# Optimization experiments

Hardware: AMD Instinct MI355X
Metric: run time of the kernel (lower is better)

## Reference

```python
import jax, jax.numpy as jnp
import numpy as np

HIDDEN = 1024
HEADS = 16
HEAD_DIM = HIDDEN // HEADS          # 64
ROT = 2 * (HEAD_DIM // 3 // 2)      # 20 (d/h/w rotary chunk), residual = 4
GRID = 256 // 16                    # crop_size // patch_size = 16
DEPTH = 16 // 2                     # frames_per_clip // tubelet_size = 8
N_VIDEO = DEPTH * GRID * GRID       # 2048
N_ACTION = 16
B = 2
SCALE = HEAD_DIM ** -0.5


def _rope(x, pos):
    # interleaved RoPE (VJEPA2 rotate_queries_or_keys): pairs (x[2i], x[2i+1])
    D = x.shape[-1]
    omega = 1.0 / (10000.0 ** (jnp.arange(D // 2, dtype=x.dtype) / (D / 2.0)))
    freq = pos.astype(x.dtype)[..., None] * omega          # (N, D/2)
    cos, sin = jnp.cos(freq), jnp.sin(freq)
    x1, x2 = x[..., 0::2], x[..., 1::2]
    return jnp.stack([x1 * cos - x2 * sin, x2 * cos + x1 * sin], axis=-1).reshape(x.shape)


def _rope3(qk, d_pos, h_pos, w_pos):
    # rotate three ROT-sized chunks (depth/height/width axes), leave residual dims as-is
    parts = [_rope(qk[..., 0:ROT], d_pos),
             _rope(qk[..., ROT:2 * ROT], h_pos),
             _rope(qk[..., 2 * ROT:3 * ROT], w_pos)]
    if 3 * ROT < HEAD_DIM:
        parts.append(qk[..., 3 * ROT:])
    return jnp.concatenate(parts, axis=-1)


def _forward(video_hidden_states, action_hidden_states, W_q, b_q, W_k, b_k, W_v, b_v,
             W_qa, b_qa, W_ka, b_ka, W_va, b_va, W_proj, b_proj, W_proj_a, b_proj_a):
    Bsz, Nv, _ = video_hidden_states.shape
    Na = action_hidden_states.shape[1]

    def proj(x, W, b):  # -> (B, H, N, Dh)
        y = x @ W.T + b
        return y.reshape(Bsz, -1, HEADS, HEAD_DIM).transpose(0, 2, 1, 3)

    qv = proj(video_hidden_states, W_q, b_q)
    kv = proj(video_hidden_states, W_k, b_k)
    vv = proj(video_hidden_states, W_v, b_v)

    # 3-axis position ids for raster-ordered video tokens
    ids = jnp.arange(Nv)
    tpf = GRID * GRID
    d_pos = ids // tpf
    rem = ids - tpf * d_pos
    h_pos = rem // GRID
    w_pos = rem - GRID * h_pos

    qv = _rope3(qv, d_pos, h_pos, w_pos)
    kv = _rope3(kv, d_pos, h_pos, w_pos)

    qa = proj(action_hidden_states, W_qa, b_qa)
    ka = proj(action_hidden_states, W_ka, b_ka)
    va = proj(action_hidden_states, W_va, b_va)

    # actions: linspace between frame-id of token 0 and token 1 (faithful to source)
    a_pos = jnp.linspace(d_pos[0].astype(jnp.float32), d_pos[1].astype(jnp.float32), Na)
    qa = _rope3(qa, a_pos, a_pos, a_pos)
    ka = _rope3(ka, a_pos, a_pos, a_pos)

    # joint attention over concatenated video+action token sequence
    q = jnp.concatenate([qv, qa], axis=2)
    k = jnp.concatenate([kv, ka], axis=2)
    v = jnp.concatenate([vv, va], axis=2)

    scores = jnp.einsum('bhqd,bhkd->bhqk', q, k) * SCALE
    probs = jax.nn.softmax(scores, axis=-1)
    ctx = jnp.einsum('bhqk,bhkd->bhqd', probs, v)
    ctx = ctx.transpose(0, 2, 1, 3).reshape(Bsz, Nv + Na, HIDDEN)

    out_video = ctx[:, :Nv] @ W_proj.T + b_proj
    out_action = ctx[:, Nv:] @ W_proj_a.T + b_proj_a
    return out_video, out_action


def setup_inputs() -> dict:
    key = jax.random.key(0)
    ks = jax.random.split(key, 12)
    sd = HIDDEN ** -0.5
    inp = {}
    for i, n in enumerate(['q', 'k', 'v', 'qa', 'ka', 'va', 'proj', 'proj_a']):
        inp[f'W_{n}'] = jax.random.normal(ks[i], (HIDDEN, HIDDEN), jnp.float32) * sd
        inp[f'b_{n}'] = jnp.zeros((HIDDEN,), jnp.float32)
    inp['video_hidden_states'] = jax.random.normal(ks[10], (B, N_VIDEO, HIDDEN), jnp.float32)
    inp['action_hidden_states'] = jax.random.normal(ks[11], (B, N_ACTION, HIDDEN), jnp.float32)
    return inp


def reference(video_hidden_states, action_hidden_states, W_q, b_q, W_k, b_k, W_v, b_v,
              W_qa, b_qa, W_ka, b_ka, W_va, b_va, W_proj, b_proj, W_proj_a, b_proj_a):
    return _forward(video_hidden_states, action_hidden_states, W_q, b_q, W_k, b_k, W_v, b_v,
                    W_qa, b_qa, W_ka, b_ka, W_va, b_va, W_proj, b_proj, W_proj_a, b_proj_a)
```

## Files before the change

### kernel.cpp

```cpp
#include <hip/hip_runtime.h>
#include <stdint.h>

#define HID   1024
#define NHEAD 16
#define HDIM  64
#define NV    2048
#define NA    16
#define NTOK  2064
#define BSZ   2
#define MROWS 4128
#define MPAD  4224
#define WSZ   1048576
#define EXP_C1 0.18033688011112042f
#define EXP_C2 16.0f

#define POFF(r,k)  (((((r)>>4)*32  + ((k)>>5))*512) + ((((k)>>3)&3)*128) + (((r)&15)*8) + ((k)&7))
#define QOFF(t,d)  (((((t)>>4)*2   + ((d)>>5))*512) + ((((d)>>3)&3)*128) + (((t)&15)*8) + ((d)&7))
#define VOFF(d,ky) (((((d)>>4)*65  + ((ky)>>5))*512) + ((((ky)>>3)&3)*128) + (((d)&15)*8) + ((ky)&7))
#define QPLANE (129*2*512)
#define VPLANE (4*65*512)

typedef __bf16 bf16x8 __attribute__((ext_vector_type(8)));
typedef unsigned short u16x8 __attribute__((ext_vector_type(8)));
typedef unsigned short u16x4 __attribute__((ext_vector_type(4)));
typedef float f32x4 __attribute__((ext_vector_type(4)));

__device__ __forceinline__ unsigned short f2bf(float f) {
  unsigned u = __builtin_bit_cast(unsigned, f);
  u += 0x7FFFu + ((u >> 16) & 1u);
  return (unsigned short)(u >> 16);
}
__device__ __forceinline__ unsigned short f2bf_trunc(float f) {
  return (unsigned short)(__builtin_bit_cast(unsigned, f) >> 16);
}
__device__ __forceinline__ bf16x8 ldfrag(const unsigned short* p) {
  return __builtin_bit_cast(bf16x8, *(const u16x8*)p);
}

__global__ __launch_bounds__(256) void cvt_kernel(
    const float* __restrict__ W0, const float* __restrict__ W1,
    const float* __restrict__ W2, const float* __restrict__ W3,
    const float* __restrict__ W4, const float* __restrict__ W5,
    const float* __restrict__ W6, const float* __restrict__ W7,
    const float* __restrict__ video, const float* __restrict__ action,
    unsigned short* __restrict__ Wb, unsigned short* __restrict__ Xp)
{
  const int y = blockIdx.y;
  const size_t idx = ((size_t)blockIdx.x * 256 + threadIdx.x) * 8;
  const float* src; unsigned short* dstbase; int row;
  if (y < 8) {
    const float* Ws[8] = {W0, W1, W2, W3, W4, W5, W6, W7};
    src = Ws[y] + idx; dstbase = Wb + (size_t)y * WSZ; row = (int)(idx >> 10);
  } else if (y < 12) {
    src = video + (size_t)(y - 8) * WSZ + idx; dstbase = Xp;
    row = ((y - 8) << 10) + (int)(idx >> 10);
  } else {
    if (idx >= (size_t)BSZ * NA * HID) return;
    src = action + idx; dstbase = Xp; row = 4096 + (int)(idx >> 10);
  }
  const int k0 = (int)(idx & 1023);
  float4 f0 = *(const float4*)src;
  float4 f1 = *(const float4*)(src + 4);
  u16x8 v;
  v[0]=f2bf(f0.x); v[1]=f2bf(f0.y); v[2]=f2bf(f0.z); v[3]=f2bf(f0.w);
  v[4]=f2bf(f1.x); v[5]=f2bf(f1.y); v[6]=f2bf(f1.z); v[7]=f2bf(f1.w);
  *(u16x8*)(dstbase + POFF(row, k0)) = v;
}

__device__ __forceinline__ void row2bt(int rg, int& b, int& tok, bool& valid) {
  if (rg < 4096) { b = rg >> 11; tok = rg & 2047; valid = true; }
  else { int t = rg - 4096; b = t >> 4; tok = 2048 + (t & 15); valid = rg < MROWS; }
}

__global__ __launch_bounds__(512) void qkv_kernel(
    const unsigned short* __restrict__ Xp, const unsigned short* __restrict__ Wb,
    const float* __restrict__ bq, const float* __restrict__ bk,
    const float* __restrict__ bv, const float* __restrict__ bqa,
    const float* __restrict__ bka, const float* __restrict__ bva,
    unsigned short* __restrict__ Qpk, unsigned short* __restrict__ Kpk,
    unsigned short* __restrict__ Vpk)
{
  const int tid  = threadIdx.x;
  const int w    = tid >> 6;
  const int lane = tid & 63;
  const int quad = lane >> 4;
  const int l16  = lane & 15;
  const int mh   = w & 3;
  const int nh   = w >> 2;
  const int n0   = blockIdx.x * 128;
  const int z    = blockIdx.y;
  const int m0   = blockIdx.z * 128;
  const bool atile = (blockIdx.z == 32);

  const unsigned short* Wz = Wb + (size_t)(atile ? 3 + z : z) * WSZ;
  const float* bias = (z == 0) ? (atile ? bqa : bq)
                    : (z == 1) ? (atile ? bka : bk)
                               : (atile ? bva : bv);

  const int Mt = (m0 >> 4) + mh * 2;
  const int Nt = (n0 >> 4) + nh * 4;
  const unsigned short* pa = Xp + (size_t)Mt * 32 * 512 + lane * 8;
  const unsigned short* pb = Wz + (size_t)Nt * 32 * 512 + lane * 8;

  f32x4 acc[2][4] = {};
  bf16x8 af[2][2], bf[2][4];

#pragma unroll
  for (int mi = 0; mi < 2; mi++) af[0][mi] = ldfrag(pa + (size_t)(mi * 32) * 512);
#pragma unroll
  for (int ni = 0; ni < 4; ni++) bf[0][ni] = ldfrag(pb + (size_t)(ni * 32) * 512);

  for (int kt = 0; kt < 32; kt++) {
    const int cb = kt & 1, nb = cb ^ 1;
    if (kt < 31) {
#pragma unroll
      for (int mi = 0; mi < 2; mi++) af[nb][mi] = ldfrag(pa + (size_t)(mi * 32 + kt + 1) * 512);
#pragma unroll
      for (int ni = 0; ni < 4; ni++) bf[nb][ni] = ldfrag(pb + (size_t)(ni * 32 + kt + 1) * 512);
    }
#pragma unroll
    for (int mi = 0; mi < 2; mi++)
#pragma unroll
      for (int ni = 0; ni < 4; ni++)
        acc[mi][ni] = __builtin_amdgcn_mfma_f32_16x16x32_bf16(af[cb][mi], bf[cb][ni], acc[mi][ni], 0, 0, 0);
  }

  if (z < 2) {
    unsigned short* O = (z == 0) ? Qpk : Kpk;
#pragma unroll
    for (int mi = 0; mi < 2; mi++) {
      const int rgb = m0 + mh * 32 + mi * 16 + quad * 4;
#pragma unroll
      for (int ni = 0; ni < 4; ni++) {
        const int gcol = n0 + nh * 64 + ni * 16 + l16;
        const int head = gcol >> 6, col = gcol & 63;
        const float bias_v = bias[gcol];
        const int seg = (col >= 40) ? 2 : (col >= 20) ? 1 : 0;
        const int tin = col - seg * 20;
        const float om = exp2f(-(float)(tin >> 1) * 1.3287712379549449f);
        const bool evn = !(tin & 1);
#pragma unroll
        for (int r = 0; r < 4; r++) {
          int rg = rgb + r;
          int b, tok; bool valid;
          row2bt(rg, b, tok, valid);
          float val = acc[mi][ni][r] + bias_v;
          float part = __shfl_xor(val, 1);
          if (tok < 2048 && col < 60) {
            int dp = tok >> 8, hp = (tok >> 4) & 15, wp = tok & 15;
            float pos = (seg == 0) ? (float)dp : (seg == 1) ? (float)hp : (float)wp;
            float fr = pos * om;
            float cs = cosf(fr), sn = sinf(fr);
            val = evn ? (val * cs - part * sn) : (val * cs + part * sn);
          }
          if (valid)
            O[(size_t)(b * NHEAD + head) * QPLANE + QOFF(tok, col)] = f2bf(val);
        }
      }
    }
  } else {
#pragma unroll
    for (int mi = 0; mi < 2; mi++) {
      const int rgb = m0 + mh * 32 + mi * 16 + quad * 4;
      int b, tok; bool valid;
      row2bt(rgb, b, tok, valid);
#pragma unroll
      for (int ni = 0; ni < 4; ni++) {
        const int gcol = n0 + nh * 64 + ni * 16 + l16;
        const int head = gcol >> 6, d = gcol & 63;
        const float bias_v = bias[gcol];
        u16x4 pk;
#pragma unroll
        for (int r = 0; r < 4; r++) pk[r] = f2bf(acc[mi][ni][r] + bias_v);
        if (valid)
          *(u16x4*)&Vpk[(size_t)(b * NHEAD + head) * VPLANE + VOFF(d, tok)] = pk;
      }
    }
  }
}

__global__ __launch_bounds__(256) void attn_kernel(
    const unsigned short* __restrict__ Qpk,
    const unsigned short* __restrict__ Kpk,
    const unsigned short* __restrict__ Vpk,
    unsigned short* __restrict__ ctxp)
{
  __shared__ unsigned short Ps[4][16][68];

  const int tid  = threadIdx.x;
  const int wave = tid >> 6;
  const int lane = tid & 63;
  const int quad = lane >> 4;
  const int l16  = lane & 15;
  const int bh   = blockIdx.x;
  const int q0   = blockIdx.y * 64;
  const unsigned short* Qp = Qpk + (size_t)bh * QPLANE + lane * 8;
  const unsigned short* Kp = Kpk + (size_t)bh * QPLANE + lane * 8;
  const unsigned short* Vp = Vpk + (size_t)bh * VPLANE + lane * 8;

  const int qt = min((q0 >> 4) + wave, 128);
  bf16x8 aq[2];
#pragma unroll
  for (int c = 0; c < 2; c++) aq[c] = ldfrag(Qp + (size_t)(qt * 2 + c) * 512);

  u16x8 ones_u;
#pragma unroll
  for (int i = 0; i < 8; i++) ones_u[i] = 0x3F80;
  const bf16x8 ones = __builtin_bit_cast(bf16x8, ones_u);

  f32x4 oacc[4] = {};
  f32x4 lacc = {};

  bf16x8 kf[8], vf[8];
#pragma unroll
  for (int f = 0; f < 8; f++) kf[f] = ldfrag(Kp + (size_t)f * 512);
#pragma unroll
  for (int nt = 0; nt < 4; nt++)
#pragma unroll
    for (int c = 0; c < 2; c++) vf[nt * 2 + c] = ldfrag(Vp + (size_t)(nt * 65 + c) * 512);

  for (int it = 0; it < 32; it++) {
    f32x4 sacc[4] = {};
#pragma unroll
    for (int nt = 0; nt < 4; nt++)
#pragma unroll
      for (int c = 0; c < 2; c++)
        sacc[nt] = __builtin_amdgcn_mfma_f32_16x16x32_bf16(aq[c], kf[nt * 2 + c], sacc[nt], 0, 0, 0);
    if (it < 31) {
#pragma unroll
      for (int f = 0; f < 8; f++) kf[f] = ldfrag(Kp + (size_t)((it + 1) * 8 + f) * 512);
    }
#pragma unroll
    for (int nt = 0; nt < 4; nt++)
#pragma unroll
      for (int rr = 0; rr < 4; rr++)
        Ps[wave][quad * 4 + rr][nt * 16 + l16] =
            f2bf_trunc(exp2f(__builtin_fmaf(sacc[nt][rr], EXP_C1, -EXP_C2)));

#pragma unroll
    for (int c = 0; c < 2; c++) {
      u16x4 alo = *(const u16x4*)&Ps[wave][l16][c * 32 + quad * 8];
      u16x4 ahi = *(const u16x4*)&Ps[wave][l16][c * 32 + quad * 8 + 4];
      bf16x8 ap = __builtin_bit_cast(bf16x8,
          __builtin_shufflevector(alo, ahi, 0, 1, 2, 3, 4, 5, 6, 7));
#pragma unroll
      for (int nt = 0; nt < 4; nt++)
        oacc[nt] = __builtin_amdgcn_mfma_f32_16x16x32_bf16(ap, vf[nt * 2 + c], oacc[nt], 0, 0, 0);
      lacc = __builtin_amdgcn_mfma_f32_16x16x32_bf16(ap, ones, lacc, 0, 0, 0);
    }
    if (it < 31) {
#pragma unroll
      for (int nt = 0; nt < 4; nt++)
#pragma unroll
        for (int c = 0; c < 2; c++)
          vf[nt * 2 + c] = ldfrag(Vp + (size_t)(nt * 65 + (it + 1) * 2 + c) * 512);
    }
  }

  {
    f32x4 s0 = {};
#pragma unroll
    for (int c = 0; c < 2; c++) {
      bf16x8 bk = ldfrag(Kp + (size_t)(128 * 2 + c) * 512);
      s0 = __builtin_amdgcn_mfma_f32_16x16x32_bf16(aq[c], bk, s0, 0, 0, 0);
    }
#pragma unroll
    for (int rr = 0; rr < 4; rr++) {
      Ps[wave][quad * 4 + rr][l16]      = f2bf_trunc(exp2f(__builtin_fmaf(s0[rr], EXP_C1, -EXP_C2)));
      Ps[wave][quad * 4 + rr][16 + l16] = 0;
    }
    u16x4 alo = *(const u16x4*)&Ps[wave][l16][quad * 8];
    u16x4 ahi = *(const u16x4*)&Ps[wave][l16][quad * 8 + 4];
    bf16x8 ap = __builtin_bit_cast(bf16x8,
        __builtin_shufflevector(alo, ahi, 0, 1, 2, 3, 4, 5, 6, 7));
#pragma unroll
    for (int nt = 0; nt < 4; nt++) {
      bf16x8 bv = ldfrag(Vp + (size_t)(nt * 65 + 64) * 512);
      oacc[nt] = __builtin_amdgcn_mfma_f32_16x16x32_bf16(ap, bv, oacc[nt], 0, 0, 0);
    }
    lacc = __builtin_amdgcn_mfma_f32_16x16x32_bf16(ap, ones, lacc, 0, 0, 0);
  }

  const int b = bh >> 4, h = bh & 15;
  float rl[4];
#pragma unroll
  for (int rr = 0; rr < 4; rr++) rl[rr] = 1.f / lacc[rr];
#pragma unroll
  for (int nt = 0; nt < 4; nt++) {
#pragma unroll
    for (int rr = 0; rr < 4; rr++) {
      int token = q0 + wave * 16 + quad * 4 + rr;
      if (token < NTOK) {
        int row = (token < 2048) ? (b * 2048 + token) : (4096 + b * NA + (token - 2048));
        int col = h * HDIM + nt * 16 + l16;
        ctxp[POFF(row, col)] = f2bf(oacc[nt][rr] * rl[rr]);
      }
    }
  }
}

__global__ __launch_bounds__(256) void proj_kernel(
    const unsigned short* __restrict__ ctxp, const unsigned short* __restrict__ Wb,
    const float* __restrict__ bp, const float* __restrict__ bpa,
    float* __restrict__ out)
{
  const int tid  = threadIdx.x;
  const int w    = tid >> 6;
  const int lane = tid & 63;
  const int quad = lane >> 4;
  const int l16  = lane & 15;
  const int mh   = w & 1;
  const int nh   = w >> 1;
  const int m0   = blockIdx.y * 64;
  const int n0   = blockIdx.x * 64;
  const bool atile = (blockIdx.y >= 64);

  const unsigned short* Wz = Wb + (size_t)(atile ? 7 : 6) * WSZ;
  const float* bias = atile ? bpa : bp;

  const int Mt = (m0 >> 4) + mh * 2;
  const int Nt = (n0 >> 4) + nh * 2;
  const unsigned short* pa = ctxp + (size_t)Mt * 32 * 512 + lane * 8;
  const unsigned short* pb = Wz + (size_t)Nt * 32 * 512 + lane * 8;

  f32x4 acc[2][2] = {};
  bf16x8 af[2][2], bf[2][2];

#pragma unroll
  for (int mi = 0; mi < 2; mi++) af[0][mi] = ldfrag(pa + (size_t)(mi * 32) * 512);
#pragma unroll
  for (int ni = 0; ni < 2; ni++) bf[0][ni] = ldfrag(pb + (size_t)(ni * 32) * 512);

  for (int kt = 0; kt < 32; kt++) {
    const int cb = kt & 1, nb = cb ^ 1;
    if (kt < 31) {
#pragma unroll
      for (int mi = 0; mi < 2; mi++) af[nb][mi] = ldfrag(pa + (size_t)(mi * 32 + kt + 1) * 512);
#pragma unroll
      for (int ni = 0; ni < 2; ni++) bf[nb][ni] = ldfrag(pb + (size_t)(ni * 32 + kt + 1) * 512);
    }
#pragma unroll
    for (int mi = 0; mi < 2; mi++)
#pragma unroll
      for (int ni = 0; ni < 2; ni++)
        acc[mi][ni] = __builtin_amdgcn_mfma_f32_16x16x32_bf16(af[cb][mi], bf[cb][ni], acc[mi][ni], 0, 0, 0);
  }

#pragma unroll
  for (int mi = 0; mi < 2; mi++) {
    const int rgb = m0 + mh * 32 + mi * 16 + quad * 4;
#pragma unroll
    for (int ni = 0; ni < 2; ni++) {
      const int gcol = n0 + nh * 32 + ni * 16 + l16;
      const float bias_v = bias[gcol];
#pragma unroll
      for (int r = 0; r < 4; r++) {
        int rg = rgb + r;
        if (rg < MROWS) out[(size_t)rg * HID + gcol] = acc[mi][ni][r] + bias_v;
      }
    }
  }
}

extern "C" void kernel_launch(void* const* d_in, const int* in_sizes, int n_in,
                              void* d_out, int out_size, void* d_ws, size_t ws_size,
                              hipStream_t stream) {
  const float* A[18];
  if (in_sizes[0] == HID * HID) {
    for (int i = 0; i < 18; i++) A[i] = (const float*)d_in[i];
  } else {
    A[16] = (const float*)d_in[0];
    A[17] = (const float*)d_in[1];
    for (int i = 0; i < 16; i++) A[i] = (const float*)d_in[i + 2];
  }
  const float *Wq = A[0], *bq = A[1], *Wk = A[2], *bk = A[3], *Wv = A[4], *bv = A[5];
  const float *Wqa = A[6], *bqa = A[7], *Wka = A[8], *bka = A[9], *Wva = A[10], *bva = A[11];
  const float *Wp = A[12], *bp = A[13], *Wpa = A[14], *bpa = A[15];
  const float *video = A[16], *action = A[17];
  float* out = (float*)d_out;

  unsigned short* Wb   = (unsigned short*)d_ws;
  unsigned short* Xp   = Wb + (size_t)8 * WSZ;
  unsigned short* Qpk  = Xp + (size_t)(MPAD / 16) * 32 * 512;
  unsigned short* Kpk  = Qpk + (size_t)32 * QPLANE;
  unsigned short* Vpk  = Kpk + (size_t)32 * QPLANE;
  unsigned short* ctxp = Vpk + (size_t)32 * VPLANE;

  dim3 g0(512, 13);
  cvt_kernel<<<g0, 256, 0, stream>>>(Wq, Wk, Wv, Wqa, Wka, Wva, Wp, Wpa,
                                     video, action, Wb, Xp);
  dim3 g1(8, 3, 33);
  qkv_kernel<<<g1, 512, 0, stream>>>(Xp, Wb, bq, bk, bv, bqa, bka, bva,
                                     Qpk, Kpk, Vpk);
  dim3 g2(BSZ * NHEAD, 33);
  attn_kernel<<<g2, 256, 0, stream>>>(Qpk, Kpk, Vpk, ctxp);
  dim3 g3(16, 66);
  proj_kernel<<<g3, 256, 0, stream>>>(ctxp, Wb, bp, bpa, out);
}
```

Baseline: 314.9 us.

## Transpose attention MFMA operands so P fragments pack directly into LDS

The attention kernel now computes S^T and O^T by swapping the MFMA A/B operands. Each lane then packs two probabilities per 32-bit word and writes them to LDS as uint2, and the PV operand is read back with a single 128-bit load instead of two 64-bit loads plus a shuffle. The epilogue stores four contiguous bf16 context values per lane rather than scalar stores. A sched_barrier is added at the end of each loop iteration, which constrains the compiler's scheduling and may limit overlap of loads with compute.

```diff
diff --git a/kernel.cpp b/kernel.cpp
--- a/kernel.cpp
+++ b/kernel.cpp
@@ -32,6 +32,10 @@
 }
 __device__ __forceinline__ unsigned short f2bf_trunc(float f) {
   return (unsigned short)(__builtin_bit_cast(unsigned, f) >> 16);
+}
+__device__ __forceinline__ unsigned pack2bf(float a, float b) {
+  return (__builtin_bit_cast(unsigned, a) >> 16) |
+         (__builtin_bit_cast(unsigned, b) & 0xFFFF0000u);
 }
 __device__ __forceinline__ bf16x8 ldfrag(const unsigned short* p) {
   return __builtin_bit_cast(bf16x8, *(const u16x8*)p);
@@ -185,7 +189,7 @@
     const unsigned short* __restrict__ Vpk,
     unsigned short* __restrict__ ctxp)
 {
-  __shared__ unsigned short Ps[4][16][68];
+  __shared__ unsigned int Pt[4][2][64][4];
 
   const int tid  = threadIdx.x;
   const int wave = tid >> 6;
@@ -222,31 +226,33 @@
   for (int it = 0; it < 32; it++) {
     f32x4 sacc[4] = {};
 #pragma unroll
-    for (int nt = 0; nt < 4; nt++)
+    for (int f = 0; f < 4; f++)
 #pragma unroll
       for (int c = 0; c < 2; c++)
-        sacc[nt] = __builtin_amdgcn_mfma_f32_16x16x32_bf16(aq[c], kf[nt * 2 + c], sacc[nt], 0, 0, 0);
+        sacc[f] = __builtin_amdgcn_mfma_f32_16x16x32_bf16(kf[f * 2 + c], aq[c], sacc[f], 0, 0, 0);
     if (it < 31) {
 #pragma unroll
       for (int f = 0; f < 8; f++) kf[f] = ldfrag(Kp + (size_t)((it + 1) * 8 + f) * 512);
     }
 #pragma unroll
-    for (int nt = 0; nt < 4; nt++)
-#pragma unroll
-      for (int rr = 0; rr < 4; rr++)
-        Ps[wave][quad * 4 + rr][nt * 16 + l16] =
-            f2bf_trunc(exp2f(__builtin_fmaf(sacc[nt][rr], EXP_C1, -EXP_C2)));
-
+    for (int f = 0; f < 4; f++) {
+      float e0 = exp2f(__builtin_fmaf(sacc[f][0], EXP_C1, -EXP_C2));
+      float e1 = exp2f(__builtin_fmaf(sacc[f][1], EXP_C1, -EXP_C2));
+      float e2 = exp2f(__builtin_fmaf(sacc[f][2], EXP_C1, -EXP_C2));
+      float e3 = exp2f(__builtin_fmaf(sacc[f][3], EXP_C1, -EXP_C2));
+      const int c  = f >> 1;
+      const int tq = (f & 1) * 2 + (quad >> 1);
+      const int j0 = (quad & 1) * 2;
+      uint2 w2; w2.x = pack2bf(e0, e1); w2.y = pack2bf(e2, e3);
+      *(uint2*)&Pt[wave][c][tq * 16 + l16][j0] = w2;
+    }
 #pragma unroll
     for (int c = 0; c < 2; c++) {
-      u16x4 alo = *(const u16x4*)&Ps[wave][l16][c * 32 + quad * 8];
-      u16x4 ahi = *(const u16x4*)&Ps[wave][l16][c * 32 + quad * 8 + 4];
-      bf16x8 ap = __builtin_bit_cast(bf16x8,
-          __builtin_shufflevector(alo, ahi, 0, 1, 2, 3, 4, 5, 6, 7));
+      bf16x8 ptf = __builtin_bit_cast(bf16x8, *(const u16x8*)&Pt[wave][c][lane][0]);
 #pragma unroll
       for (int nt = 0; nt < 4; nt++)
-        oacc[nt] = __builtin_amdgcn_mfma_f32_16x16x32_bf16(ap, vf[nt * 2 + c], oacc[nt], 0, 0, 0);
-      lacc = __builtin_amdgcn_mfma_f32_16x16x32_bf16(ap, ones, lacc, 0, 0, 0);
+        oacc[nt] = __builtin_amdgcn_mfma_f32_16x16x32_bf16(vf[nt * 2 + c], ptf, oacc[nt], 0, 0, 0);
+      lacc = __builtin_amdgcn_mfma_f32_16x16x32_bf16(ones, ptf, lacc, 0, 0, 0);
     }
     if (it < 31) {
 #pragma unroll
@@ -255,6 +261,7 @@
         for (int c = 0; c < 2; c++)
           vf[nt * 2 + c] = ldfrag(Vp + (size_t)(nt * 65 + (it + 1) * 2 + c) * 512);
     }
+    __builtin_amdgcn_sched_barrier(0);
   }
 
   {
@@ -262,39 +269,40 @@
 #pragma unroll
     for (int c = 0; c < 2; c++) {
       bf16x8 bk = ldfrag(Kp + (size_t)(128 * 2 + c) * 512);
-      s0 = __builtin_amdgcn_mfma_f32_16x16x32_bf16(aq[c], bk, s0, 0, 0, 0);
-    }
-#pragma unroll
-    for (int rr = 0; rr < 4; rr++) {
-      Ps[wave][quad * 4 + rr][l16]      = f2bf_trunc(exp2f(__builtin_fmaf(s0[rr], EXP_C1, -EXP_C2)));
-      Ps[wave][quad * 4 + rr][16 + l16] = 0;
-    }
-    u16x4 alo = *(const u16x4*)&Ps[wave][l16][quad * 8];
-    u16x4 ahi = *(const u16x4*)&Ps[wave][l16][quad * 8 + 4];
-    bf16x8 ap = __builtin_bit_cast(bf16x8,
-        __builtin_shufflevector(alo, ahi, 0, 1, 2, 3, 4, 5, 6, 7));
+      s0 = __builtin_amdgcn_mfma_f32_16x16x32_bf16(bk, aq[c], s0, 0, 0, 0);
+    }
+    *(uint2*)&Pt[wave][0][32 + (lane >> 1)][(lane & 1) * 2] = make_uint2(0u, 0u);
+    {
+      float e0 = exp2f(__builtin_fmaf(s0[0], EXP_C1, -EXP_C2));
+      float e1 = exp2f(__builtin_fmaf(s0[1], EXP_C1, -EXP_C2));
+      float e2 = exp2f(__builtin_fmaf(s0[2], EXP_C1, -EXP_C2));
+      float e3 = exp2f(__builtin_fmaf(s0[3], EXP_C1, -EXP_C2));
+      const int tq = quad >> 1;
+      const int j0 = (quad & 1) * 2;
+      uint2 w2; w2.x = pack2bf(e0, e1); w2.y = pack2bf(e2, e3);
+      *(uint2*)&Pt[wave][0][tq * 16 + l16][j0] = w2;
+    }
+    bf16x8 ptf = __builtin_bit_cast(bf16x8, *(const u16x8*)&Pt[wave][0][lane][0]);
 #pragma unroll
     for (int nt = 0; nt < 4; nt++) {
       bf16x8 bv = ldfrag(Vp + (size_t)(nt * 65 + 64) * 512);
-      oacc[nt] = __builtin_amdgcn_mfma_f32_16x16x32_bf16(ap, bv, oacc[nt], 0, 0, 0);
-    }
-    lacc = __builtin_amdgcn_mfma_f32_16x16x32_bf16(ap, ones, lacc, 0, 0, 0);
+      oacc[nt] = __builtin_amdgcn_mfma_f32_16x16x32_bf16(bv, ptf, oacc[nt], 0, 0, 0);
+    }
+    lacc = __builtin_amdgcn_mfma_f32_16x16x32_bf16(ones, ptf, lacc, 0, 0, 0);
   }
 
   const int b = bh >> 4, h = bh & 15;
-  float rl[4];
-#pragma unroll
-  for (int rr = 0; rr < 4; rr++) rl[rr] = 1.f / lacc[rr];
-#pragma unroll
-  for (int nt = 0; nt < 4; nt++) {
-#pragma unroll
-    for (int rr = 0; rr < 4; rr++) {
-      int token = q0 + wave * 16 + quad * 4 + rr;
-      if (token < NTOK) {
-        int row = (token < 2048) ? (b * 2048 + token) : (4096 + b * NA + (token - 2048));
-        int col = h * HDIM + nt * 16 + l16;
-        ctxp[POFF(row, col)] = f2bf(oacc[nt][rr] * rl[rr]);
-      }
+  const float rl = 1.f / lacc[0];
+  const int token = q0 + wave * 16 + l16;
+  if (token < NTOK) {
+    const int row = (token < 2048) ? (b * 2048 + token) : (4096 + b * NA + (token - 2048));
+#pragma unroll
+    for (int nt = 0; nt < 4; nt++) {
+      const int col = h * HDIM + nt * 16 + quad * 4;
+      u16x4 pk;
+#pragma unroll
+      for (int r = 0; r < 4; r++) pk[r] = f2bf(oacc[nt][r] * rl);
+      *(u16x4*)&ctxp[POFF(row, col)] = pk;
     }
   }
 }
```

Measured after the change: 314.0 us. About the same (-0.3%).
